# Performance work log

Measured on AMD Instinct MI355X. Metric: run time of the kernel, lower is better.

Reference implementation:

```python
import jax, jax.numpy as jnp
import numpy as np
import math

H = 4          # n_heads
LAM = 2.0      # gate_lambda
EPS = 1e-6


def _evid_gate(t, W, b):
    # t: [B,T,d] -> g: [B,T,1] via Normal-Inverse-Gamma evidential gate
    h = t @ W.T + b                                  # [B,T,4]
    mu, v_raw, a_raw, b_raw = jnp.split(h, 4, axis=-1)
    v = jax.nn.softplus(v_raw) + EPS
    alpha = jax.nn.softplus(a_raw) + 1.0 + EPS
    beta = jax.nn.softplus(b_raw) + EPS
    var_ep = beta / (v * (alpha - 1.0))
    g = jax.nn.sigmoid(mu) * jnp.exp(-LAM * var_ep)
    return jnp.maximum(g, 1e-6)


def _ln(t, g, b):
    m = jnp.mean(t, axis=-1, keepdims=True)
    v = jnp.var(t, axis=-1, keepdims=True)
    return (t - m) / jnp.sqrt(v + 1e-5) * g + b


def _split(t):
    B, T, d = t.shape
    return t.reshape(B, T, H, d // H).transpose(0, 2, 1, 3)  # [B,H,T,dk]


def _merge(t):
    B, h, T, dk = t.shape
    return t.transpose(0, 2, 1, 3).reshape(B, T, h * dk)


def _gated_attn(q, k, v, lg_q, lg_k, mask_k, dk):
    # q:[B,H,Tq,dk], k/v:[B,H,Tk,dk], lg_q:[B,Tq], lg_k:[B,Tk], mask_k:[B,Tk] bool
    s = jnp.einsum('bhqd,bhkd->bhqk', q, k) / math.sqrt(dk)
    s = s + lg_q[:, None, :, None] + lg_k[:, None, None, :]
    s = jnp.where(mask_k[:, None, None, :], s, -jnp.inf)
    a = jax.nn.softmax(s, axis=-1)                   # dropout is identity in eval
    return jnp.einsum('bhqk,bhkd->bhqd', a, v)


def setup_inputs():
    key = jax.random.key(0)
    ks = jax.random.split(key, 20)
    B, Nx, Ny, d = 16, 512, 1024, 256
    s = 0.02
    w = lambda k, shape: jax.random.normal(k, shape, jnp.float32) * s
    return {
        'x': jax.random.normal(ks[0], (B, Nx, d), jnp.float32),
        'y': jax.random.normal(ks[1], (B, Ny, d), jnp.float32),
        'x_mask': jnp.ones((B, Nx), bool),
        'y_mask': jnp.ones((B, Ny), bool),
        'Wqx': w(ks[2], (d, d)), 'Wkx': w(ks[3], (d, d)), 'Wvx': w(ks[4], (d, d)),
        'Wqy': w(ks[5], (d, d)), 'Wky': w(ks[6], (d, d)), 'Wvy': w(ks[7], (d, d)),
        'gWx': w(ks[8], (4, d)), 'gbx': jnp.zeros((4,), jnp.float32),
        'gWy': w(ks[9], (4, d)), 'gby': jnp.zeros((4,), jnp.float32),
        'Wox': w(ks[10], (d, d)), 'Woy': w(ks[11], (d, d)),
        'lnx_g': jnp.ones((d,), jnp.float32), 'lnx_b': jnp.zeros((d,), jnp.float32),
        'lny_g': jnp.ones((d,), jnp.float32), 'lny_b': jnp.zeros((d,), jnp.float32),
        'ffx_W': w(ks[12], (d, d)), 'ffx_b': jnp.zeros((d,), jnp.float32),
        'ffy_W': w(ks[13], (d, d)), 'ffy_b': jnp.zeros((d,), jnp.float32),
    }


def reference(x, y, x_mask, y_mask, Wqx, Wkx, Wvx, Wqy, Wky, Wvy,
              gWx, gbx, gWy, gby, Wox, Woy,
              lnx_g, lnx_b, lny_g, lny_b, ffx_W, ffx_b, ffy_W, ffy_b):
    d = x.shape[-1]
    dk = d // H
    qx, kx, vx = _split(x @ Wqx.T), _split(x @ Wkx.T), _split(x @ Wvx.T)
    qy, ky, vy = _split(y @ Wqy.T), _split(y @ Wky.T), _split(y @ Wvy.T)
    gx = _evid_gate(x, gWx, gbx)                     # [B,Nx,1]
    gy = _evid_gate(y, gWy, gby)                     # [B,Ny,1]
    lgx = jnp.log(gx)[..., 0]                        # [B,Nx]
    lgy = jnp.log(gy)[..., 0]                        # [B,Ny]

    out_x = _merge(_gated_attn(qx, ky, vy, lgx, lgy, y_mask, dk)) @ Wox.T
    x2 = _ln(x + out_x, lnx_g, lnx_b)
    x2 = _ln(x2 + jax.nn.silu(x2 @ ffx_W.T + ffx_b), lnx_g, lnx_b)

    out_y = _merge(_gated_attn(qy, kx, vx, lgy, lgx, x_mask, dk)) @ Woy.T
    y2 = _ln(y + out_y, lny_g, lny_b)
    y2 = _ln(y2 + jax.nn.silu(y2 @ ffy_W.T + ffy_b), lny_g, lny_b)

    return x2, y2, gx[..., 0], gy[..., 0]
```

## Files before the change

kernel.cpp:

```cpp
#include <hip/hip_runtime.h>
#include <stdint.h>

typedef unsigned short u16;
typedef unsigned int   u32;
typedef __attribute__((ext_vector_type(8))) short bf16x8;
typedef __attribute__((ext_vector_type(4))) float f32x4;

__device__ __forceinline__ u16 f2b(float f) {
    union { float f; u32 i; } v; v.f = f;
    return (u16)((v.i + 0x7fffu + ((v.i >> 16) & 1u)) >> 16);
}
__device__ __forceinline__ float b2f(u16 u) {
    union { float f; u32 i; } v; v.i = ((u32)u) << 16; return v.f;
}
__device__ __forceinline__ bf16x8 pack8(const float* s) {
    union { bf16x8 v; u16 u[8]; } r;
    #pragma unroll
    for (int i = 0; i < 8; i++) r.u[i] = f2b(s[i]);
    return r.v;
}
__device__ __forceinline__ float softplus_f(float x) {
    return x > 15.f ? x : log1pf(__expf(x));
}

__global__ __launch_bounds__(256) void prep(
    const float* __restrict__ X, const float* __restrict__ Y,
    const float* __restrict__ gWx, const float* __restrict__ gbx,
    const float* __restrict__ gWy, const float* __restrict__ gby,
    float* __restrict__ goutx, float* __restrict__ lgx,
    float* __restrict__ gouty, float* __restrict__ lgy,
    u16* __restrict__ xb, u16* __restrict__ yb,
    const float* p0, const float* p1, const float* p2, const float* p3,
    const float* p4, const float* p5, const float* p6, const float* p7,
    const float* p8, const float* p9, u16* __restrict__ wdst)
{
    const int blk = blockIdx.x;
    const int t = threadIdx.x;
    if (blk < 3072) {
        int g = blk * 256 + t;
        const bool isx = g < 262144;
        const float* src; u16* dst; size_t off; int tok;
        const float *gW, *gb; float *go, *lg;
        if (isx) {
            src = X; dst = xb; off = (size_t)g * 8; tok = g >> 5;
            gW = gWx; gb = gbx; go = goutx; lg = lgx;
        } else {
            int g2 = g - 262144;
            src = Y; dst = yb; off = (size_t)g2 * 8; tok = g2 >> 5;
            gW = gWy; gb = gby; go = gouty; lg = lgy;
        }
        float tmp[8];
        *(float4*)&tmp[0] = *(const float4*)(src + off);
        *(float4*)&tmp[4] = *(const float4*)(src + off + 4);
        *(bf16x8*)(dst + off) = pack8(tmp);

        const int c0 = (t & 31) * 8;
        float a[4];
        #pragma unroll
        for (int j = 0; j < 4; j++) {
            float4 w0 = *(const float4*)(gW + j * 256 + c0);
            float4 w1 = *(const float4*)(gW + j * 256 + c0 + 4);
            a[j] = tmp[0]*w0.x + tmp[1]*w0.y + tmp[2]*w0.z + tmp[3]*w0.w
                 + tmp[4]*w1.x + tmp[5]*w1.y + tmp[6]*w1.z + tmp[7]*w1.w;
        }
        #pragma unroll
        for (int o = 16; o > 0; o >>= 1) {
            #pragma unroll
            for (int j = 0; j < 4; j++) a[j] += __shfl_xor(a[j], o);
        }
        if ((t & 31) == 0) {
            float mu    = a[0] + gb[0];
            float v     = softplus_f(a[1] + gb[1]) + 1e-6f;
            float alpha = softplus_f(a[2] + gb[2]) + 1.0f + 1e-6f;
            float beta  = softplus_f(a[3] + gb[3]) + 1e-6f;
            float var_ep = beta / (v * (alpha - 1.0f));
            float sig = 1.0f / (1.0f + __expf(-mu));
            float gg = fmaxf(sig * __expf(-2.0f * var_ep), 1e-6f);
            go[tok] = gg;
            lg[tok] = log2f(gg);
        }
    } else {
        int g = (blk - 3072) * 256 + t;
        int wsel = g >> 13, off = g & 8191;
        const float* src;
        switch (wsel) {
            case 0: src = p0; break; case 1: src = p1; break;
            case 2: src = p2; break; case 3: src = p3; break;
            case 4: src = p4; break; case 5: src = p5; break;
            case 6: src = p6; break; case 7: src = p7; break;
            case 8: src = p8; break; default: src = p9; break;
        }
        float tmp[8];
        *(float4*)&tmp[0] = *(const float4*)(src + (size_t)off * 8);
        *(float4*)&tmp[4] = *(const float4*)(src + (size_t)off * 8 + 4);
        *(bf16x8*)(wdst + ((size_t)wsel * 65536) + (size_t)off * 8) = pack8(tmp);
    }
}

__global__ __launch_bounds__(256, 2) void gemm_qkv(
    const u16* __restrict__ Axb, const u16* __restrict__ Ayb,
    const u16* __restrict__ Wx, const u16* __restrict__ Wy,
    u16* __restrict__ Qx, u16* __restrict__ Kx, u16* __restrict__ VTx,
    u16* __restrict__ Qy, u16* __restrict__ Ky, u16* __restrict__ VTy)
{
    __shared__ short smem[2 * 128 * 72];
    short* As = smem;
    short* Ws = smem + 128 * 72;
    const int t = threadIdx.x;
    const int id = blockIdx.x;
    const int wk = (id & 7) * 144 + (id >> 3);
    const int bn = wk % 6;
    int bm = wk / 6;
    const bool isx = bm < 64;
    const u16* A  = isx ? Axb : Ayb;
    const u16* W  = isx ? Wx : Wy;
    u16* Qo  = isx ? Qx : Qy;
    u16* Ko  = isx ? Kx : Ky;
    u16* VTo = isx ? VTx : VTy;
    const int tqsh = isx ? 9 : 10;
    if (!isx) bm -= 64;

    const int w = t >> 6, lane = t & 63, li = lane & 15, quad = lane >> 4;
    const int wm = (w >> 1) * 64, wn = (w & 1) * 64;
    const int sr = t >> 1, scb = (t & 1) * 32;

    f32x4 zero = {0.f, 0.f, 0.f, 0.f};
    f32x4 acc[4][4];
    #pragma unroll
    for (int a = 0; a < 4; a++)
        #pragma unroll
        for (int b = 0; b < 4; b++) acc[a][b] = zero;

    for (int ch = 0; ch < 4; ch++) {
        const int k0 = ch * 64;
        if (ch) __syncthreads();
        {
            const u16* Ap = A + (size_t)(bm * 128 + sr) * 256 + k0 + scb;
            const u16* Wp = W + (size_t)(bn * 128 + sr) * 256 + k0 + scb;
            #pragma unroll
            for (int j = 0; j < 4; j++) {
                *(uint4*)&As[sr * 72 + scb + j * 8] = *(const uint4*)(Ap + j * 8);
                *(uint4*)&Ws[sr * 72 + scb + j * 8] = *(const uint4*)(Wp + j * 8);
            }
        }
        __syncthreads();
        #pragma unroll
        for (int c = 0; c < 2; c++) {
            bf16x8 af[4], bf[4];
            #pragma unroll
            for (int mt = 0; mt < 4; mt++)
                af[mt] = *(const bf16x8*)&As[(wm + mt * 16 + li) * 72 + c * 32 + quad * 8];
            #pragma unroll
            for (int nt = 0; nt < 4; nt++)
                bf[nt] = *(const bf16x8*)&Ws[(wn + nt * 16 + li) * 72 + c * 32 + quad * 8];
            #pragma unroll
            for (int mt = 0; mt < 4; mt++)
                #pragma unroll
                for (int nt = 0; nt < 4; nt++)
                    acc[mt][nt] = __builtin_amdgcn_mfma_f32_16x16x32_bf16(
                        af[mt], bf[nt], acc[mt][nt], 0, 0, 0);
        }
    }

    const int sel = bn >> 1;
    if (sel < 2) {
        u16* Co = (sel == 0) ? Qo : Ko;
        __syncthreads();
        short* Lin = smem;
        #pragma unroll
        for (int nt = 0; nt < 4; nt++) {
            const int cl = wn + nt * 16 + li;
            #pragma unroll
            for (int mt = 0; mt < 4; mt++) {
                const int rl0 = wm + mt * 16 + quad * 4;
                #pragma unroll
                for (int i = 0; i < 4; i++)
                    Lin[(rl0 + i) * 136 + cl] = (short)f2b(acc[mt][nt][i]);
            }
        }
        __syncthreads();
        const int dl = t >> 1, seg = t & 1;
        const int cb = (bn & 1) * 128 + seg * 64;
        u16* dst = Co + (size_t)(bm * 128 + dl) * 256 + cb;
        #pragma unroll
        for (int k = 0; k < 8; k++)
            *(uint4*)(dst + k * 8) = *(const uint4*)&Lin[dl * 136 + seg * 64 + k * 8];
    } else {
        __syncthreads();
        short* Trans = smem;
        #pragma unroll
        for (int nt = 0; nt < 4; nt++) {
            const int cl = wn + nt * 16 + li;
            #pragma unroll
            for (int mt = 0; mt < 4; mt++) {
                const int rl0 = wm + mt * 16 + quad * 4;
                #pragma unroll
                for (int i = 0; i < 4; i++)
                    Trans[cl * 136 + rl0 + i] = (short)f2b(acc[mt][nt][i]);
            }
        }
        __syncthreads();
        const int dl = t >> 1, seg = t & 1;
        const int col = (bn - 4) * 128 + dl;
        const int h = col >> 6, dd = col & 63;
        const int bz = (bm * 128) >> tqsh;
        const int key0 = (bm * 128) & ((1 << tqsh) - 1);
        u16* dst = VTo + ((((size_t)(bz * 4 + h)) * 64 + dd) << tqsh) + key0 + seg * 64;
        #pragma unroll
        for (int k = 0; k < 8; k++)
            *(uint4*)(dst + k * 8) = *(const uint4*)&Trans[dl * 136 + seg * 64 + k * 8];
    }
}

__global__ __launch_bounds__(256, 3) void attn3(
    const u16* __restrict__ Q1, const u16* __restrict__ K1, const u16* __restrict__ VT1,
    const float* __restrict__ LG1, u16* __restrict__ O1,
    const u16* __restrict__ Q2, const u16* __restrict__ K2, const u16* __restrict__ VT2,
    const float* __restrict__ LG2, u16* __restrict__ O2)
{
    __shared__ short Ks[64][72];
    __shared__ short VTs[64][72];
    __shared__ short Ps[128][72];
    __shared__ float Lk[64];

    const int t = threadIdx.x;
    const int id = blockIdx.x;
    const int wk = (id & 7) * 96 + (id >> 3);
    const int xi = wk % 12;
    const int rest = wk / 12;
    const int h = rest & 3;
    const int bz = rest >> 2;
    const bool ph1 = xi < 4;
    const int qtl = ph1 ? xi : xi - 4;
    const u16* Q  = ph1 ? Q1 : Q2;
    const u16* K  = ph1 ? K1 : K2;
    const u16* VT = ph1 ? VT1 : VT2;
    const float* LG = ph1 ? LG1 : LG2;
    u16* O = ph1 ? O1 : O2;
    const int Tq = ph1 ? 512 : 1024;
    const int Tk = ph1 ? 1024 : 512;

    const int w = t >> 6, lane = t & 63, li = lane & 15, quad = lane >> 4;
    const int q0 = qtl * 128;

    bf16x8 qf[2][2];
    #pragma unroll
    for (int s = 0; s < 2; s++) {
        const u16* qp = Q + (size_t)(bz * Tq + q0 + s * 64 + w * 16 + li) * 256 + h * 64 + quad * 8;
        qf[s][0] = *(const bf16x8*)qp;
        qf[s][1] = *(const bf16x8*)(qp + 32);
    }

    float lsum[2] = {0.f, 0.f};
    f32x4 zero = {0.f, 0.f, 0.f, 0.f};
    f32x4 oacc[2][4];
    #pragma unroll
    for (int s = 0; s < 2; s++)
        #pragma unroll
        for (int md = 0; md < 4; md++) oacc[s][md] = zero;

    const int sr = t >> 2, sc = (t & 3) * 16;
    const u16* Kp  = K + (size_t)(bz * Tk + sr) * 256 + h * 64 + sc;
    const u16* VTp = VT + ((size_t)(bz * 4 + h) * 64 + sr) * Tk + sc;
    const float* LGp = LG + (size_t)bz * Tk;

    uint4 pk0, pk1, pv0, pv1;
    float plk;
    pk0 = *(const uint4*)(Kp);
    pk1 = *(const uint4*)(Kp + 8);
    pv0 = *(const uint4*)(VTp);
    pv1 = *(const uint4*)(VTp + 8);
    plk = (t < 64) ? LGp[t] : 0.f;

    const float SCL = 0.18033688f;

    for (int kt = 0; kt < Tk; kt += 64) {
        __syncthreads();
        *(uint4*)&Ks[sr][sc]      = pk0;
        *(uint4*)&Ks[sr][sc + 8]  = pk1;
        *(uint4*)&VTs[sr][sc]     = pv0;
        *(uint4*)&VTs[sr][sc + 8] = pv1;
        if (t < 64) Lk[t] = plk;
        __syncthreads();
        if (kt + 64 < Tk) {
            pk0 = *(const uint4*)(Kp + (size_t)(kt + 64) * 256);
            pk1 = *(const uint4*)(Kp + (size_t)(kt + 64) * 256 + 8);
            pv0 = *(const uint4*)(VTp + kt + 64);
            pv1 = *(const uint4*)(VTp + kt + 64 + 8);
            if (t < 64) plk = LGp[kt + 64 + t];
        }

        #pragma unroll
        for (int s = 0; s < 2; s++) {
            f32x4 sacc[4] = {zero, zero, zero, zero};
            #pragma unroll
            for (int c = 0; c < 2; c++)
                #pragma unroll
                for (int mt = 0; mt < 4; mt++) {
                    bf16x8 af = *(const bf16x8*)&Ks[mt * 16 + li][c * 32 + quad * 8];
                    sacc[mt] = __builtin_amdgcn_mfma_f32_16x16x32_bf16(af, qf[s][c], sacc[mt], 0, 0, 0);
                }
            #pragma unroll
            for (int mt = 0; mt < 4; mt++) {
                float4 lk4 = *(const float4*)&Lk[mt * 16 + quad * 4];
                float x0 = fmaf(sacc[mt][0], SCL, lk4.x);
                float x1 = fmaf(sacc[mt][1], SCL, lk4.y);
                float x2 = fmaf(sacc[mt][2], SCL, lk4.z);
                float x3 = fmaf(sacc[mt][3], SCL, lk4.w);
                float p0, p1, p2, p3;
                asm("v_exp_f32 %0, %1" : "=v"(p0) : "v"(x0));
                asm("v_exp_f32 %0, %1" : "=v"(p1) : "v"(x1));
                asm("v_exp_f32 %0, %1" : "=v"(p2) : "v"(x2));
                asm("v_exp_f32 %0, %1" : "=v"(p3) : "v"(x3));
                lsum[s] += (p0 + p1) + (p2 + p3);
                u32 lo, hi;
                asm("v_cvt_pk_bf16_f32 %0, %1, %2" : "=v"(lo) : "v"(p0), "v"(p1));
                asm("v_cvt_pk_bf16_f32 %0, %1, %2" : "=v"(hi) : "v"(p2), "v"(p3));
                uint2 st; st.x = lo; st.y = hi;
                *(uint2*)&Ps[s * 64 + w * 16 + li][mt * 16 + quad * 4] = st;
            }
        }

        #pragma unroll
        for (int c = 0; c < 2; c++) {
            bf16x8 vf[4], pf[2];
            #pragma unroll
            for (int md = 0; md < 4; md++)
                vf[md] = *(const bf16x8*)&VTs[md * 16 + li][c * 32 + quad * 8];
            #pragma unroll
            for (int s = 0; s < 2; s++)
                pf[s] = *(const bf16x8*)&Ps[s * 64 + w * 16 + li][c * 32 + quad * 8];
            #pragma unroll
            for (int s = 0; s < 2; s++)
                #pragma unroll
                for (int md = 0; md < 4; md++)
                    oacc[s][md] = __builtin_amdgcn_mfma_f32_16x16x32_bf16(
                        vf[md], pf[s], oacc[s][md], 0, 0, 0);
        }
    }

    #pragma unroll
    for (int s = 0; s < 2; s++) {
        float l = lsum[s];
        l += __shfl_xor(l, 16);
        l += __shfl_xor(l, 32);
        const float inv = 1.0f / l;
        u16* op = O + (size_t)(bz * Tq + q0 + s * 64 + w * 16 + li) * 256 + h * 64;
        #pragma unroll
        for (int md = 0; md < 4; md++) {
            float o0 = oacc[s][md][0] * inv;
            float o1 = oacc[s][md][1] * inv;
            float o2 = oacc[s][md][2] * inv;
            float o3 = oacc[s][md][3] * inv;
            u32 lo, hi;
            asm("v_cvt_pk_bf16_f32 %0, %1, %2" : "=v"(lo) : "v"(o0), "v"(o1));
            asm("v_cvt_pk_bf16_f32 %0, %1, %2" : "=v"(hi) : "v"(o2), "v"(o3));
            uint2 st; st.x = lo; st.y = hi;
            *(uint2*)(op + md * 16 + quad * 4) = st;
        }
    }
}

__global__ __launch_bounds__(256, 3) void gemm_ffln(
    const u16* __restrict__ Axb, const u16* __restrict__ Ayb,
    const u16* __restrict__ W1x, const u16* __restrict__ W1y,
    const u16* __restrict__ W2x, const u16* __restrict__ W2y,
    const float* __restrict__ fbx, const float* __restrict__ fby,
    const float* __restrict__ Rx, const float* __restrict__ Ry,
    const float* __restrict__ gxv, const float* __restrict__ bxv,
    const float* __restrict__ gyv, const float* __restrict__ byv,
    float* __restrict__ Fx, float* __restrict__ Fy)
{
    __shared__ short Ws[256 * 40];
    __shared__ short A2[32 * 264];
    __shared__ float Sred[32][4];
    __shared__ float Ssq[32][4];

    const int t = threadIdx.x;
    int blk = blockIdx.x;
    const bool isx = blk < 256;
    const u16* A  = isx ? Axb : Ayb;
    const u16* W1 = isx ? W1x : W1y;
    const u16* W2 = isx ? W2x : W2y;
    const float* fb    = isx ? fbx : fby;
    const float* RES   = isx ? Rx : Ry;
    const float* gamma = isx ? gxv : gyv;
    const float* beta  = isx ? bxv : byv;
    float* F = isx ? Fx : Fy;
    if (!isx) blk -= 256;
    const int r0 = blk * 32;

    const int w = t >> 6, lane = t & 63, li = lane & 15, quad = lane >> 4;
    const int wn = w * 64;

    {
        const int ar = t >> 3;
        const int ac = (t & 7) * 32;
        const u16* Ap = A + (size_t)(r0 + ar) * 256 + ac;
        #pragma unroll
        for (int j = 0; j < 4; j++)
            *(uint4*)&A2[ar * 264 + ac + j * 8] = *(const uint4*)(Ap + j * 8);
    }

    f32x4 zero = {0.f, 0.f, 0.f, 0.f};
    f32x4 acc[2][4];
    #pragma unroll
    for (int a = 0; a < 2; a++)
        #pragma unroll
        for (int b = 0; b < 4; b++) acc[a][b] = zero;

    const int wr = t >> 2;
    const int wc = (t & 3) * 8;

    for (int ch = 0; ch < 8; ch++) {
        const int k0 = ch * 32;
        if (ch) __syncthreads();
        #pragma unroll
        for (int jj = 0; jj < 4; jj++) {
            const int row = wr + jj * 64;
            *(uint4*)&Ws[row * 40 + wc] = *(const uint4*)(W1 + (size_t)row * 256 + k0 + wc);
        }
        __syncthreads();
        bf16x8 af[2], bf[4];
        #pragma unroll
        for (int mt = 0; mt < 2; mt++)
            af[mt] = *(const bf16x8*)&A2[(mt * 16 + li) * 264 + k0 + quad * 8];
        #pragma unroll
        for (int nt = 0; nt < 4; nt++)
            bf[nt] = *(const bf16x8*)&Ws[(wn + nt * 16 + li) * 40 + quad * 8];
        #pragma unroll
        for (int mt = 0; mt < 2; mt++)
            #pragma unroll
            for (int nt = 0; nt < 4; nt++)
                acc[mt][nt] = __builtin_amdgcn_mfma_f32_16x16x32_bf16(
                    af[mt], bf[nt], acc[mt][nt], 0, 0, 0);
    }

    float gv[4], btv[4], fbv[4];
    #pragma unroll
    for (int nt = 0; nt < 4; nt++) {
        const int col = wn + nt * 16 + li;
        gv[nt]  = gamma[col];
        btv[nt] = beta[col];
        fbv[nt] = fb[col];
    }

    float psum[2][4], psq[2][4];
    #pragma unroll
    for (int mt = 0; mt < 2; mt++) {
        #pragma unroll
        for (int i = 0; i < 4; i++) { psum[mt][i] = 0.f; psq[mt][i] = 0.f; }
        #pragma unroll
        for (int nt = 0; nt < 4; nt++) {
            const int col = wn + nt * 16 + li;
            #pragma unroll
            for (int i = 0; i < 4; i++) {
                const int row = mt * 16 + quad * 4 + i;
                float v = acc[mt][nt][i] + RES[(size_t)(r0 + row) * 256 + col];
                acc[mt][nt][i] = v;
                psum[mt][i] += v;
                psq[mt][i]  += v * v;
            }
        }
        #pragma unroll
        for (int i = 0; i < 4; i++) {
            #pragma unroll
            for (int off = 1; off < 16; off <<= 1) {
                psum[mt][i] += __shfl_xor(psum[mt][i], off);
                psq[mt][i]  += __shfl_xor(psq[mt][i], off);
            }
        }
    }
    if (li == 0) {
        #pragma unroll
        for (int mt = 0; mt < 2; mt++)
            #pragma unroll
            for (int i = 0; i < 4; i++) {
                Sred[mt * 16 + quad * 4 + i][w] = psum[mt][i];
                Ssq[mt * 16 + quad * 4 + i][w]  = psq[mt][i];
            }
    }
    __syncthreads();

    #pragma unroll
    for (int mt = 0; mt < 2; mt++) {
        #pragma unroll
        for (int i = 0; i < 4; i++) {
            const int row = mt * 16 + quad * 4 + i;
            float4 s4 = *(const float4*)&Sred[row][0];
            float4 q4 = *(const float4*)&Ssq[row][0];
            float S  = (s4.x + s4.y) + (s4.z + s4.w);
            float S2 = (q4.x + q4.y) + (q4.z + q4.w);
            float mean = S * (1.0f / 256.0f);
            float var  = S2 * (1.0f / 256.0f) - mean * mean;
            float rstd = rsqrtf(var + 1e-5f);
            #pragma unroll
            for (int nt = 0; nt < 4; nt++) {
                const int col = wn + nt * 16 + li;
                float ln = (acc[mt][nt][i] - mean) * rstd * gv[nt] + btv[nt];
                acc[mt][nt][i] = ln;
                A2[row * 264 + col] = (short)f2b(ln);
            }
        }
    }

    f32x4 acc2[2][4];
    #pragma unroll
    for (int a = 0; a < 2; a++)
        #pragma unroll
        for (int b = 0; b < 4; b++) acc2[a][b] = zero;

    for (int ch = 0; ch < 8; ch++) {
        const int k0 = ch * 32;
        __syncthreads();
        #pragma unroll
        for (int jj = 0; jj < 4; jj++) {
            const int row = wr + jj * 64;
            *(uint4*)&Ws[row * 40 + wc] = *(const uint4*)(W2 + (size_t)row * 256 + k0 + wc);
        }
        __syncthreads();
        bf16x8 af[2], bf[4];
        #pragma unroll
        for (int mt = 0; mt < 2; mt++)
            af[mt] = *(const bf16x8*)&A2[(mt * 16 + li) * 264 + k0 + quad * 8];
        #pragma unroll
        for (int nt = 0; nt < 4; nt++)
            bf[nt] = *(const bf16x8*)&Ws[(wn + nt * 16 + li) * 40 + quad * 8];
        #pragma unroll
        for (int mt = 0; mt < 2; mt++)
            #pragma unroll
            for (int nt = 0; nt < 4; nt++)
                acc2[mt][nt] = __builtin_amdgcn_mfma_f32_16x16x32_bf16(
                    af[mt], bf[nt], acc2[mt][nt], 0, 0, 0);
    }

    #pragma unroll
    for (int mt = 0; mt < 2; mt++) {
        #pragma unroll
        for (int i = 0; i < 4; i++) { psum[mt][i] = 0.f; psq[mt][i] = 0.f; }
        #pragma unroll
        for (int nt = 0; nt < 4; nt++) {
            #pragma unroll
            for (int i = 0; i < 4; i++) {
                float u = acc2[mt][nt][i] + fbv[nt];
                u = u / (1.f + __expf(-u));
                u += acc[mt][nt][i];
                acc2[mt][nt][i] = u;
                psum[mt][i] += u;
                psq[mt][i]  += u * u;
            }
        }
        #pragma unroll
        for (int i = 0; i < 4; i++) {
            #pragma unroll
            for (int off = 1; off < 16; off <<= 1) {
                psum[mt][i] += __shfl_xor(psum[mt][i], off);
                psq[mt][i]  += __shfl_xor(psq[mt][i], off);
            }
        }
    }
    if (li == 0) {
        #pragma unroll
        for (int mt = 0; mt < 2; mt++)
            #pragma unroll
            for (int i = 0; i < 4; i++) {
                Sred[mt * 16 + quad * 4 + i][w] = psum[mt][i];
                Ssq[mt * 16 + quad * 4 + i][w]  = psq[mt][i];
            }
    }
    __syncthreads();

    #pragma unroll
    for (int mt = 0; mt < 2; mt++) {
        #pragma unroll
        for (int i = 0; i < 4; i++) {
            const int row = mt * 16 + quad * 4 + i;
            float4 s4 = *(const float4*)&Sred[row][0];
            float4 q4 = *(const float4*)&Ssq[row][0];
            float S  = (s4.x + s4.y) + (s4.z + s4.w);
            float S2 = (q4.x + q4.y) + (q4.z + q4.w);
            float mean = S * (1.0f / 256.0f);
            float var  = S2 * (1.0f / 256.0f) - mean * mean;
            float rstd = rsqrtf(var + 1e-5f);
            #pragma unroll
            for (int nt = 0; nt < 4; nt++) {
                const int col = wn + nt * 16 + li;
                F[(size_t)(r0 + row) * 256 + col] =
                    (acc2[mt][nt][i] - mean) * rstd * gv[nt] + btv[nt];
            }
        }
    }
}

extern "C" void kernel_launch(void* const* d_in, const int* in_sizes, int n_in,
                              void* d_out, int out_size, void* d_ws, size_t ws_size,
                              hipStream_t stream)
{
    const float* x = (const float*)d_in[0];
    const float* y = (const float*)d_in[1];
    const int wb = (n_in >= 24) ? 4 : 2;
    const float* Wqx  = (const float*)d_in[wb + 0];
    const float* Wkx  = (const float*)d_in[wb + 1];
    const float* Wvx  = (const float*)d_in[wb + 2];
    const float* Wqy  = (const float*)d_in[wb + 3];
    const float* Wky  = (const float*)d_in[wb + 4];
    const float* Wvy  = (const float*)d_in[wb + 5];
    const float* gWx  = (const float*)d_in[wb + 6];
    const float* gbx  = (const float*)d_in[wb + 7];
    const float* gWy  = (const float*)d_in[wb + 8];
    const float* gby  = (const float*)d_in[wb + 9];
    const float* Wox  = (const float*)d_in[wb + 10];
    const float* Woy  = (const float*)d_in[wb + 11];
    const float* lnxg = (const float*)d_in[wb + 12];
    const float* lnxb = (const float*)d_in[wb + 13];
    const float* lnyg = (const float*)d_in[wb + 14];
    const float* lnyb = (const float*)d_in[wb + 15];
    const float* ffxW = (const float*)d_in[wb + 16];
    const float* ffxb = (const float*)d_in[wb + 17];
    const float* ffyW = (const float*)d_in[wb + 18];
    const float* ffyb = (const float*)d_in[wb + 19];

    char* ws = (char*)d_ws;
    float* lgx = (float*)(ws);
    float* lgy = (float*)(ws + 32768);
    u16* wbf   = (u16*)(ws + 98304);
    u16* xbf   = (u16*)(ws + 1409024);
    u16* ybf   = xbf + (size_t)8192 * 256;
    u16* qb    = ybf + (size_t)16384 * 256;
    u16* kb    = qb  + (size_t)8192 * 256;
    u16* vtb   = kb  + (size_t)16384 * 256;
    u16* qb2   = vtb + (size_t)16384 * 256;
    u16* kb2   = qb2 + (size_t)16384 * 256;
    u16* vtb2  = kb2 + (size_t)8192 * 256;
    u16* ctxx  = vtb2 + (size_t)8192 * 256;
    u16* ctxy  = ctxx + (size_t)8192 * 256;

    float* out_x2 = (float*)d_out;
    float* out_y2 = out_x2 + 2097152;
    float* out_gx = out_x2 + 6291456;
    float* out_gy = out_x2 + 6299648;

    prep<<<3392, 256, 0, stream>>>(
        x, y, gWx, gbx, gWy, gby, out_gx, lgx, out_gy, lgy,
        xbf, ybf,
        Wqx, Wkx, Wvx, Wqy, Wky, Wvy, Wox, Woy, ffxW, ffyW, wbf);
    gemm_qkv<<<dim3(1152), 256, 0, stream>>>(
        xbf, ybf, wbf + 0 * 65536, wbf + 3 * 65536,
        qb, kb2, vtb2, qb2, kb, vtb);
    attn3<<<dim3(768), 256, 0, stream>>>(
        qb, kb, vtb, lgy, ctxx, qb2, kb2, vtb2, lgx, ctxy);
    gemm_ffln<<<768, 256, 0, stream>>>(
        ctxx, ctxy, wbf + 6 * 65536, wbf + 7 * 65536,
        wbf + 8 * 65536, wbf + 9 * 65536,
        ffxb, ffyb, x, y,
        lnxg, lnxb, lnyg, lnyb, out_x2, out_y2);

    (void)in_sizes; (void)out_size; (void)ws_size;
}
```

Before: 210.5 us.

## Halve attention query tile to double blocks and widen FFN weight chunks

The attention kernel now handles 64 query rows per block instead of 128, doubling the grid to 1536 blocks, shrinking the P shared buffer and register accumulators, and raising launch bounds to 5 waves per SIMD for more occupancy. The cost is that each K/V tile is loaded into shared memory twice as often relative to the compute done on it. Separately, the FFN/LN GEMM stages weights in 64-wide K chunks instead of 32, halving the number of barrier-separated chunk loads at the price of more LDS per block.

```diff
diff --git a/kernel.cpp b/kernel.cpp
--- a/kernel.cpp
+++ b/kernel.cpp
@@ -212,7 +212,7 @@
     }
 }
 
-__global__ __launch_bounds__(256, 3) void attn3(
+__global__ __launch_bounds__(256, 5) void attn3(
     const u16* __restrict__ Q1, const u16* __restrict__ K1, const u16* __restrict__ VT1,
     const float* __restrict__ LG1, u16* __restrict__ O1,
     const u16* __restrict__ Q2, const u16* __restrict__ K2, const u16* __restrict__ VT2,
@@ -220,18 +220,18 @@
 {
     __shared__ short Ks[64][72];
     __shared__ short VTs[64][72];
-    __shared__ short Ps[128][72];
+    __shared__ short Ps[64][72];
     __shared__ float Lk[64];
 
     const int t = threadIdx.x;
     const int id = blockIdx.x;
-    const int wk = (id & 7) * 96 + (id >> 3);
-    const int xi = wk % 12;
-    const int rest = wk / 12;
+    const int wk = (id & 7) * 192 + (id >> 3);
+    const int xi = wk % 24;
+    const int rest = wk / 24;
     const int h = rest & 3;
     const int bz = rest >> 2;
-    const bool ph1 = xi < 4;
-    const int qtl = ph1 ? xi : xi - 4;
+    const bool ph1 = xi < 8;
+    const int qtl = ph1 ? xi : xi - 8;
     const u16* Q  = ph1 ? Q1 : Q2;
     const u16* K  = ph1 ? K1 : K2;
     const u16* VT = ph1 ? VT1 : VT2;
@@ -241,23 +241,20 @@
     const int Tk = ph1 ? 1024 : 512;
 
     const int w = t >> 6, lane = t & 63, li = lane & 15, quad = lane >> 4;
-    const int q0 = qtl * 128;
-
-    bf16x8 qf[2][2];
-    #pragma unroll
-    for (int s = 0; s < 2; s++) {
-        const u16* qp = Q + (size_t)(bz * Tq + q0 + s * 64 + w * 16 + li) * 256 + h * 64 + quad * 8;
-        qf[s][0] = *(const bf16x8*)qp;
-        qf[s][1] = *(const bf16x8*)(qp + 32);
-    }
-
-    float lsum[2] = {0.f, 0.f};
+    const int q0 = qtl * 64;
+
+    bf16x8 qf[2];
+    {
+        const u16* qp = Q + (size_t)(bz * Tq + q0 + w * 16 + li) * 256 + h * 64 + quad * 8;
+        qf[0] = *(const bf16x8*)qp;
+        qf[1] = *(const bf16x8*)(qp + 32);
+    }
+
+    float lsum = 0.f;
     f32x4 zero = {0.f, 0.f, 0.f, 0.f};
-    f32x4 oacc[2][4];
-    #pragma unroll
-    for (int s = 0; s < 2; s++)
-        #pragma unroll
-        for (int md = 0; md < 4; md++) oacc[s][md] = zero;
+    f32x4 oacc[4];
+    #pragma unroll
+    for (int md = 0; md < 4; md++) oacc[md] = zero;
 
     const int sr = t >> 2, sc = (t & 3) * 16;
     const u16* Kp  = K + (size_t)(bz * Tk + sr) * 256 + h * 64 + sc;
@@ -290,68 +287,60 @@
             if (t < 64) plk = LGp[kt + 64 + t];
         }
 
-        #pragma unroll
-        for (int s = 0; s < 2; s++) {
-            f32x4 sacc[4] = {zero, zero, zero, zero};
-            #pragma unroll
-            for (int c = 0; c < 2; c++)
-                #pragma unroll
-                for (int mt = 0; mt < 4; mt++) {
-                    bf16x8 af = *(const bf16x8*)&Ks[mt * 16 + li][c * 32 + quad * 8];
-                    sacc[mt] = __builtin_amdgcn_mfma_f32_16x16x32_bf16(af, qf[s][c], sacc[mt], 0, 0, 0);
-                }
+        f32x4 sacc[4] = {zero, zero, zero, zero};
+        #pragma unroll
+        for (int c = 0; c < 2; c++)
             #pragma unroll
             for (int mt = 0; mt < 4; mt++) {
-                float4 lk4 = *(const float4*)&Lk[mt * 16 + quad * 4];
-                float x0 = fmaf(sacc[mt][0], SCL, lk4.x);
-                float x1 = fmaf(sacc[mt][1], SCL, lk4.y);
-                float x2 = fmaf(sacc[mt][2], SCL, lk4.z);
-                float x3 = fmaf(sacc[mt][3], SCL, lk4.w);
-                float p0, p1, p2, p3;
-                asm("v_exp_f32 %0, %1" : "=v"(p0) : "v"(x0));
-                asm("v_exp_f32 %0, %1" : "=v"(p1) : "v"(x1));
-                asm("v_exp_f32 %0, %1" : "=v"(p2) : "v"(x2));
-                asm("v_exp_f32 %0, %1" : "=v"(p3) : "v"(x3));
-                lsum[s] += (p0 + p1) + (p2 + p3);
-                u32 lo, hi;
-                asm("v_cvt_pk_bf16_f32 %0, %1, %2" : "=v"(lo) : "v"(p0), "v"(p1));
-                asm("v_cvt_pk_bf16_f32 %0, %1, %2" : "=v"(hi) : "v"(p2), "v"(p3));
-                uint2 st; st.x = lo; st.y = hi;
-                *(uint2*)&Ps[s * 64 + w * 16 + li][mt * 16 + quad * 4] = st;
-            }
+                bf16x8 af = *(const bf16x8*)&Ks[mt * 16 + li][c * 32 + quad * 8];
+                sacc[mt] = __builtin_amdgcn_mfma_f32_16x16x32_bf16(af, qf[c], sacc[mt], 0, 0, 0);
+            }
+        #pragma unroll
+        for (int mt = 0; mt < 4; mt++) {
+            float4 lk4 = *(const float4*)&Lk[mt * 16 + quad * 4];
+            float x0 = fmaf(sacc[mt][0], SCL, lk4.x);
+            float x1 = fmaf(sacc[mt][1], SCL, lk4.y);
+            float x2 = fmaf(sacc[mt][2], SCL, lk4.z);
+            float x3 = fmaf(sacc[mt][3], SCL, lk4.w);
+            float p0, p1, p2, p3;
+            asm("v_exp_f32 %0, %1" : "=v"(p0) : "v"(x0));
+            asm("v_exp_f32 %0, %1" : "=v"(p1) : "v"(x1));
+            asm("v_exp_f32 %0, %1" : "=v"(p2) : "v"(x2));
+            asm("v_exp_f32 %0, %1" : "=v"(p3) : "v"(x3));
+            lsum += (p0 + p1) + (p2 + p3);
+            u32 lo, hi;
+            asm("v_cvt_pk_bf16_f32 %0, %1, %2" : "=v"(lo) : "v"(p0), "v"(p1));
+            asm("v_cvt_pk_bf16_f32 %0, %1, %2" : "=v"(hi) : "v"(p2), "v"(p3));
+            uint2 st; st.x = lo; st.y = hi;
+            *(uint2*)&Ps[w * 16 + li][mt * 16 + quad * 4] = st;
         }
 
         #pragma unroll
         for (int c = 0; c < 2; c++) {
-            bf16x8 vf[4], pf[2];
+            bf16x8 vf[4];
             #pragma unroll
             for (int md = 0; md < 4; md++)
                 vf[md] = *(const bf16x8*)&VTs[md * 16 + li][c * 32 + quad * 8];
-            #pragma unroll
-            for (int s = 0; s < 2; s++)
-                pf[s] = *(const bf16x8*)&Ps[s * 64 + w * 16 + li][c * 32 + quad * 8];
-            #pragma unroll
-            for (int s = 0; s < 2; s++)
-                #pragma unroll
-                for (int md = 0; md < 4; md++)
-                    oacc[s][md] = __builtin_amdgcn_mfma_f32_16x16x32_bf16(
-                        vf[md], pf[s], oacc[s][md], 0, 0, 0);
-        }
-    }
-
-    #pragma unroll
-    for (int s = 0; s < 2; s++) {
-        float l = lsum[s];
+            bf16x8 pfv = *(const bf16x8*)&Ps[w * 16 + li][c * 32 + quad * 8];
+            #pragma unroll
+            for (int md = 0; md < 4; md++)
+                oacc[md] = __builtin_amdgcn_mfma_f32_16x16x32_bf16(
+                    vf[md], pfv, oacc[md], 0, 0, 0);
+        }
+    }
+
+    {
+        float l = lsum;
         l += __shfl_xor(l, 16);
         l += __shfl_xor(l, 32);
         const float inv = 1.0f / l;
-        u16* op = O + (size_t)(bz * Tq + q0 + s * 64 + w * 16 + li) * 256 + h * 64;
+        u16* op = O + (size_t)(bz * Tq + q0 + w * 16 + li) * 256 + h * 64;
         #pragma unroll
         for (int md = 0; md < 4; md++) {
-            float o0 = oacc[s][md][0] * inv;
-            float o1 = oacc[s][md][1] * inv;
-            float o2 = oacc[s][md][2] * inv;
-            float o3 = oacc[s][md][3] * inv;
+            float o0 = oacc[md][0] * inv;
+            float o1 = oacc[md][1] * inv;
+            float o2 = oacc[md][2] * inv;
+            float o3 = oacc[md][3] * inv;
             u32 lo, hi;
             asm("v_cvt_pk_bf16_f32 %0, %1, %2" : "=v"(lo) : "v"(o0), "v"(o1));
             asm("v_cvt_pk_bf16_f32 %0, %1, %2" : "=v"(hi) : "v"(o2), "v"(o3));
@@ -371,7 +360,7 @@
     const float* __restrict__ gyv, const float* __restrict__ byv,
     float* __restrict__ Fx, float* __restrict__ Fy)
 {
-    __shared__ short Ws[256 * 40];
+    __shared__ short Ws[256 * 68];
     __shared__ short A2[32 * 264];
     __shared__ float Sred[32][4];
     __shared__ float Ssq[32][4];
@@ -409,31 +398,34 @@
         #pragma unroll
         for (int b = 0; b < 4; b++) acc[a][b] = zero;
 
-    const int wr = t >> 2;
-    const int wc = (t & 3) * 8;
-
-    for (int ch = 0; ch < 8; ch++) {
-        const int k0 = ch * 32;
+    const int wr0 = t >> 3, wseg = (t & 7) * 8;
+
+    for (int ch = 0; ch < 4; ch++) {
+        const int k0 = ch * 64;
         if (ch) __syncthreads();
         #pragma unroll
-        for (int jj = 0; jj < 4; jj++) {
-            const int row = wr + jj * 64;
-            *(uint4*)&Ws[row * 40 + wc] = *(const uint4*)(W1 + (size_t)row * 256 + k0 + wc);
-        }
-        __syncthreads();
-        bf16x8 af[2], bf[4];
-        #pragma unroll
-        for (int mt = 0; mt < 2; mt++)
-            af[mt] = *(const bf16x8*)&A2[(mt * 16 + li) * 264 + k0 + quad * 8];
-        #pragma unroll
-        for (int nt = 0; nt < 4; nt++)
-            bf[nt] = *(const bf16x8*)&Ws[(wn + nt * 16 + li) * 40 + quad * 8];
-        #pragma unroll
-        for (int mt = 0; mt < 2; mt++)
+        for (int jj = 0; jj < 8; jj++) {
+            const int row = wr0 + jj * 32;
+            *(uint4*)&Ws[row * 68 + wseg] =
+                *(const uint4*)(W1 + (size_t)row * 256 + k0 + wseg);
+        }
+        __syncthreads();
+        #pragma unroll
+        for (int c = 0; c < 2; c++) {
+            bf16x8 af[2], bf[4];
+            #pragma unroll
+            for (int mt = 0; mt < 2; mt++)
+                af[mt] = *(const bf16x8*)&A2[(mt * 16 + li) * 264 + k0 + c * 32 + quad * 8];
             #pragma unroll
             for (int nt = 0; nt < 4; nt++)
-                acc[mt][nt] = __builtin_amdgcn_mfma_f32_16x16x32_bf16(
-                    af[mt], bf[nt], acc[mt][nt], 0, 0, 0);
+                bf[nt] = *(const bf16x8*)&Ws[(wn + nt * 16 + li) * 68 + c * 32 + quad * 8];
+            #pragma unroll
+            for (int mt = 0; mt < 2; mt++)
+                #pragma unroll
+                for (int nt = 0; nt < 4; nt++)
+                    acc[mt][nt] = __builtin_amdgcn_mfma_f32_16x16x32_bf16(
+                        af[mt], bf[nt], acc[mt][nt], 0, 0, 0);
+        }
     }
 
     float gv[4], btv[4], fbv[4];
@@ -510,28 +502,32 @@
         #pragma unroll
         for (int b = 0; b < 4; b++) acc2[a][b] = zero;
 
-    for (int ch = 0; ch < 8; ch++) {
-        const int k0 = ch * 32;
-        __syncthreads();
-        #pragma unroll
-        for (int jj = 0; jj < 4; jj++) {
-            const int row = wr + jj * 64;
-            *(uint4*)&Ws[row * 40 + wc] = *(const uint4*)(W2 + (size_t)row * 256 + k0 + wc);
-        }
-        __syncthreads();
-        bf16x8 af[2], bf[4];
-        #pragma unroll
-        for (int mt = 0; mt < 2; mt++)
-            af[mt] = *(const bf16x8*)&A2[(mt * 16 + li) * 264 + k0 + quad * 8];
-        #pragma unroll
-        for (int nt = 0; nt < 4; nt++)
-            bf[nt] = *(const bf16x8*)&Ws[(wn + nt * 16 + li) * 40 + quad * 8];
-        #pragma unroll
-        for (int mt = 0; mt < 2; mt++)
+    for (int ch = 0; ch < 4; ch++) {
+        const int k0 = ch * 64;
+        __syncthreads();
+        #pragma unroll
+        for (int jj = 0; jj < 8; jj++) {
+            const int row = wr0 + jj * 32;
+            *(uint4*)&Ws[row * 68 + wseg] =
+                *(const uint4*)(W2 + (size_t)row * 256 + k0 + wseg);
+        }
+        __syncthreads();
+        #pragma unroll
+        for (int c = 0; c < 2; c++) {
+            bf16x8 af[2], bf[4];
+            #pragma unroll
+            for (int mt = 0; mt < 2; mt++)
+                af[mt] = *(const bf16x8*)&A2[(mt * 16 + li) * 264 + k0 + c * 32 + quad * 8];
             #pragma unroll
             for (int nt = 0; nt < 4; nt++)
-                acc2[mt][nt] = __builtin_amdgcn_mfma_f32_16x16x32_bf16(
-                    af[mt], bf[nt], acc2[mt][nt], 0, 0, 0);
+                bf[nt] = *(const bf16x8*)&Ws[(wn + nt * 16 + li) * 68 + c * 32 + quad * 8];
+            #pragma unroll
+            for (int mt = 0; mt < 2; mt++)
+                #pragma unroll
+                for (int nt = 0; nt < 4; nt++)
+                    acc2[mt][nt] = __builtin_amdgcn_mfma_f32_16x16x32_bf16(
+                        af[mt], bf[nt], acc2[mt][nt], 0, 0, 0);
+        }
     }
 
     #pragma unroll
@@ -647,7 +643,7 @@
     gemm_qkv<<<dim3(1152), 256, 0, stream>>>(
         xbf, ybf, wbf + 0 * 65536, wbf + 3 * 65536,
         qb, kb2, vtb2, qb2, kb, vtb);
-    attn3<<<dim3(768), 256, 0, stream>>>(
+    attn3<<<dim3(1536), 256, 0, stream>>>(
         qb, kb, vtb, lgy, ctxx, qb2, kb2, vtb2, lgx, ctxy);
     gemm_ffln<<<768, 256, 0, stream>>>(
         ctxx, ctxy, wbf + 6 * 65536, wbf + 7 * 65536,
```

After: 217.1 us. +3.1%, slower.

## Add MFMA wave priority in attention and widen FF-GEMM K chunks to 64

Applied to the files above, without the earlier changes.

The attention kernel now raises wave priority with s_setprio around the QK and PV MFMA blocks, so the matrix core stays fed while other waves do the exp and LDS work. The fused FF/LayerNorm GEMM now stages 64-wide K chunks of the weight matrix instead of 32, with a padded stride of 68, which halves the number of load/barrier rounds. The cost is more LDS per block, which may reduce occupancy under the 3-blocks-per-CU launch bound.

```diff
diff --git a/kernel.cpp b/kernel.cpp
--- a/kernel.cpp
+++ b/kernel.cpp
@@ -293,6 +293,7 @@
         #pragma unroll
         for (int s = 0; s < 2; s++) {
             f32x4 sacc[4] = {zero, zero, zero, zero};
+            __builtin_amdgcn_s_setprio(1);
             #pragma unroll
             for (int c = 0; c < 2; c++)
                 #pragma unroll
@@ -300,6 +301,7 @@
                     bf16x8 af = *(const bf16x8*)&Ks[mt * 16 + li][c * 32 + quad * 8];
                     sacc[mt] = __builtin_amdgcn_mfma_f32_16x16x32_bf16(af, qf[s][c], sacc[mt], 0, 0, 0);
                 }
+            __builtin_amdgcn_s_setprio(0);
             #pragma unroll
             for (int mt = 0; mt < 4; mt++) {
                 float4 lk4 = *(const float4*)&Lk[mt * 16 + quad * 4];
@@ -321,6 +323,7 @@
             }
         }
 
+        __builtin_amdgcn_s_setprio(1);
         #pragma unroll
         for (int c = 0; c < 2; c++) {
             bf16x8 vf[4], pf[2];
@@ -337,6 +340,7 @@
                     oacc[s][md] = __builtin_amdgcn_mfma_f32_16x16x32_bf16(
                         vf[md], pf[s], oacc[s][md], 0, 0, 0);
         }
+        __builtin_amdgcn_s_setprio(0);
     }
 
     #pragma unroll
@@ -371,7 +375,7 @@
     const float* __restrict__ gyv, const float* __restrict__ byv,
     float* __restrict__ Fx, float* __restrict__ Fy)
 {
-    __shared__ short Ws[256 * 40];
+    __shared__ short Ws[256 * 68];
     __shared__ short A2[32 * 264];
     __shared__ float Sred[32][4];
     __shared__ float Ssq[32][4];
@@ -409,31 +413,34 @@
         #pragma unroll
         for (int b = 0; b < 4; b++) acc[a][b] = zero;
 
-    const int wr = t >> 2;
-    const int wc = (t & 3) * 8;
-
-    for (int ch = 0; ch < 8; ch++) {
-        const int k0 = ch * 32;
+    const int wr0 = t >> 3, wseg = (t & 7) * 8;
+
+    for (int ch = 0; ch < 4; ch++) {
+        const int k0 = ch * 64;
         if (ch) __syncthreads();
         #pragma unroll
-        for (int jj = 0; jj < 4; jj++) {
-            const int row = wr + jj * 64;
-            *(uint4*)&Ws[row * 40 + wc] = *(const uint4*)(W1 + (size_t)row * 256 + k0 + wc);
-        }
-        __syncthreads();
-        bf16x8 af[2], bf[4];
-        #pragma unroll
-        for (int mt = 0; mt < 2; mt++)
-            af[mt] = *(const bf16x8*)&A2[(mt * 16 + li) * 264 + k0 + quad * 8];
-        #pragma unroll
-        for (int nt = 0; nt < 4; nt++)
-            bf[nt] = *(const bf16x8*)&Ws[(wn + nt * 16 + li) * 40 + quad * 8];
-        #pragma unroll
-        for (int mt = 0; mt < 2; mt++)
+        for (int jj = 0; jj < 8; jj++) {
+            const int row = wr0 + jj * 32;
+            *(uint4*)&Ws[row * 68 + wseg] =
+                *(const uint4*)(W1 + (size_t)row * 256 + k0 + wseg);
+        }
+        __syncthreads();
+        #pragma unroll
+        for (int c = 0; c < 2; c++) {
+            bf16x8 af[2], bf[4];
+            #pragma unroll
+            for (int mt = 0; mt < 2; mt++)
+                af[mt] = *(const bf16x8*)&A2[(mt * 16 + li) * 264 + k0 + c * 32 + quad * 8];
             #pragma unroll
             for (int nt = 0; nt < 4; nt++)
-                acc[mt][nt] = __builtin_amdgcn_mfma_f32_16x16x32_bf16(
-                    af[mt], bf[nt], acc[mt][nt], 0, 0, 0);
+                bf[nt] = *(const bf16x8*)&Ws[(wn + nt * 16 + li) * 68 + c * 32 + quad * 8];
+            #pragma unroll
+            for (int mt = 0; mt < 2; mt++)
+                #pragma unroll
+                for (int nt = 0; nt < 4; nt++)
+                    acc[mt][nt] = __builtin_amdgcn_mfma_f32_16x16x32_bf16(
+                        af[mt], bf[nt], acc[mt][nt], 0, 0, 0);
+        }
     }
 
     float gv[4], btv[4], fbv[4];
@@ -510,28 +517,32 @@
         #pragma unroll
         for (int b = 0; b < 4; b++) acc2[a][b] = zero;
 
-    for (int ch = 0; ch < 8; ch++) {
-        const int k0 = ch * 32;
-        __syncthreads();
-        #pragma unroll
-        for (int jj = 0; jj < 4; jj++) {
-            const int row = wr + jj * 64;
-            *(uint4*)&Ws[row * 40 + wc] = *(const uint4*)(W2 + (size_t)row * 256 + k0 + wc);
-        }
-        __syncthreads();
-        bf16x8 af[2], bf[4];
-        #pragma unroll
-        for (int mt = 0; mt < 2; mt++)
-            af[mt] = *(const bf16x8*)&A2[(mt * 16 + li) * 264 + k0 + quad * 8];
-        #pragma unroll
-        for (int nt = 0; nt < 4; nt++)
-            bf[nt] = *(const bf16x8*)&Ws[(wn + nt * 16 + li) * 40 + quad * 8];
-        #pragma unroll
-        for (int mt = 0; mt < 2; mt++)
+    for (int ch = 0; ch < 4; ch++) {
+        const int k0 = ch * 64;
+        __syncthreads();
+        #pragma unroll
+        for (int jj = 0; jj < 8; jj++) {
+            const int row = wr0 + jj * 32;
+            *(uint4*)&Ws[row * 68 + wseg] =
+                *(const uint4*)(W2 + (size_t)row * 256 + k0 + wseg);
+        }
+        __syncthreads();
+        #pragma unroll
+        for (int c = 0; c < 2; c++) {
+            bf16x8 af[2], bf[4];
+            #pragma unroll
+            for (int mt = 0; mt < 2; mt++)
+                af[mt] = *(const bf16x8*)&A2[(mt * 16 + li) * 264 + k0 + c * 32 + quad * 8];
             #pragma unroll
             for (int nt = 0; nt < 4; nt++)
-                acc2[mt][nt] = __builtin_amdgcn_mfma_f32_16x16x32_bf16(
-                    af[mt], bf[nt], acc2[mt][nt], 0, 0, 0);
+                bf[nt] = *(const bf16x8*)&Ws[(wn + nt * 16 + li) * 68 + c * 32 + quad * 8];
+            #pragma unroll
+            for (int mt = 0; mt < 2; mt++)
+                #pragma unroll
+                for (int nt = 0; nt < 4; nt++)
+                    acc2[mt][nt] = __builtin_amdgcn_mfma_f32_16x16x32_bf16(
+                        af[mt], bf[nt], acc2[mt][nt], 0, 0, 0);
+        }
     }
 
     #pragma unroll
```

After: 212.2 us. No clear change (+0.8%).
